# Kernel optimization log

Hardware: AMD Instinct MI355X
Metric: run time of the kernel (lower is better)

Reference implementation:

```python
import jax, jax.numpy as jnp
import numpy as np

B, S, D, H = 2, 2048, 1024, 16
DQ = D // H
EPS = 1e-5


def setup_inputs() -> dict:
    key = jax.random.key(0)
    ks = jax.random.split(key, 6)
    scale = 0.02
    return {
        "x": jax.random.normal(ks[0], (B, S, D), dtype=jnp.float32),
        "ln_g": jnp.ones((D,), dtype=jnp.float32),
        "ln_b": jnp.zeros((D,), dtype=jnp.float32),
        "Wq": jax.random.normal(ks[1], (D, D), dtype=jnp.float32) * scale,
        "bq": jnp.zeros((D,), dtype=jnp.float32),
        "Wk": jax.random.normal(ks[2], (D, D), dtype=jnp.float32) * scale,
        "bk": jnp.zeros((D,), dtype=jnp.float32),
        "Wv": jax.random.normal(ks[3], (D, D), dtype=jnp.float32) * scale,
        "bv": jnp.zeros((D,), dtype=jnp.float32),
        "Wo": jax.random.normal(ks[4], (D, D), dtype=jnp.float32) * scale,
        "bo": jnp.zeros((D,), dtype=jnp.float32),
    }


def reference(x, ln_g, ln_b, Wq, bq, Wk, bk, Wv, bv, Wo, bo):
    # pre-LayerNorm (torch default eps=1e-5, biased variance)
    mu = jnp.mean(x, axis=-1, keepdims=True)
    var = jnp.mean((x - mu) ** 2, axis=-1, keepdims=True)
    xn = (x - mu) * jax.lax.rsqrt(var + EPS) * ln_g + ln_b

    # QKV projections; weights stored [d_in, d_out]
    q = xn @ Wq + bq  # [B,S,D]
    k = xn @ Wk + bk
    v = xn @ Wv + bv

    # split heads -> [B,H,S,DQ]
    def heads(t):
        return t.reshape(B, S, H, DQ).transpose(0, 2, 1, 3)
    q, k, v = heads(q), heads(k), heads(v)

    scores = jnp.einsum("bhqd,bhkd->bhqk", q, k) / jnp.sqrt(jnp.float32(DQ))
    causal = jnp.tril(jnp.ones((S, S), dtype=bool))  # True = keep
    scores = jnp.where(causal, scores, -jnp.inf)
    probs = jax.nn.softmax(scores, axis=-1)
    attn = jnp.einsum("bhqk,bhkd->bhqd", probs, v)  # [B,H,S,DQ]

    # merge heads: [B,H,S,DQ] -> [B,S,H*DQ] (matches transpose/flatten/transpose)
    merged = attn.transpose(0, 2, 1, 3).reshape(B, S, D)
    out = merged @ Wo + bo
    return out + x
```

## Files before the change

kernel.cpp:

```cpp
#include <hip/hip_runtime.h>
#include <math.h>

#define BB 2
#define SS 2048
#define DD 1024
#define HH 16
#define DQK 64
#define NROWS (BB * SS)
#define NE ((size_t)BB * SS * DD)

using short8 = __attribute__((ext_vector_type(8))) short;
using f32x4  = __attribute__((ext_vector_type(4))) float;

__device__ __forceinline__ ushort f2bf(float f) {
  union { float f; unsigned u; } c; c.f = f;
  return (ushort)((c.u + 0x7fffu + ((c.u >> 16) & 1u)) >> 16);
}

__device__ __forceinline__ unsigned cvt_pk_bf16(float lo, float hi) {
  unsigned r;
  asm("v_cvt_pk_bf16_f32 %0, %1, %2" : "=v"(r) : "v"(lo), "v"(hi));
  return r;
}

__device__ __forceinline__ f32x4 mfma16(short8 a, short8 b, f32x4 c) {
  return __builtin_amdgcn_mfma_f32_16x16x32_bf16(a, b, c, 0, 0, 0);
}

typedef __attribute__((address_space(1))) const unsigned gas_u32;
typedef __attribute__((address_space(3))) unsigned las_u32;
__device__ __forceinline__ void gload_lds16(const void* g, void* l) {
  __builtin_amdgcn_global_load_lds((gas_u32*)g, (las_u32*)l, 16, 0, 0);
}

__global__ __launch_bounds__(256) void ln_fwd(const float* __restrict__ x,
                                              const float* __restrict__ g,
                                              const float* __restrict__ bta,
                                              ushort* __restrict__ xn) {
  const int row = blockIdx.x;
  const int t = threadIdx.x;
  float4 v = ((const float4*)(x + (size_t)row * DD))[t];
  float s  = v.x + v.y + v.z + v.w;
  float ss = v.x * v.x + v.y * v.y + v.z * v.z + v.w * v.w;
#pragma unroll
  for (int off = 32; off > 0; off >>= 1) {
    s  += __shfl_xor(s, off);
    ss += __shfl_xor(ss, off);
  }
  __shared__ float red[8];
  const int wid = t >> 6, lane = t & 63;
  if (lane == 0) { red[wid] = s; red[4 + wid] = ss; }
  __syncthreads();
  const float stot  = red[0] + red[1] + red[2] + red[3];
  const float sstot = red[4] + red[5] + red[6] + red[7];
  const float mu  = stot * (1.0f / DD);
  const float var = sstot * (1.0f / DD) - mu * mu;
  const float inv = rsqrtf(var + 1e-5f);
  const float4 g4 = ((const float4*)g)[t];
  const float4 b4 = ((const float4*)bta)[t];
  ushort4 o;
  o.x = f2bf((v.x - mu) * inv * g4.x + b4.x);
  o.y = f2bf((v.y - mu) * inv * g4.y + b4.y);
  o.z = f2bf((v.z - mu) * inv * g4.z + b4.z);
  o.w = f2bf((v.w - mu) * inv * g4.w + b4.w);
  ((ushort4*)(xn + (size_t)row * DD))[t] = o;
}

__global__ __launch_bounds__(256) void wtrans(const float* __restrict__ Wq,
                                              const float* __restrict__ Wk,
                                              const float* __restrict__ Wv,
                                              const float* __restrict__ Wo,
                                              ushort* __restrict__ wt) {
  const int z = blockIdx.z;
  const float* W = (z == 0) ? Wq : (z == 1) ? Wk : (z == 2) ? Wv : Wo;
  ushort* dst = wt + (size_t)z * DD * DD;
  __shared__ float tile[64][65];
  const int t = threadIdx.x;
  const int k0 = blockIdx.x * 64, n0 = blockIdx.y * 64;
  const int tr = t >> 4, tc = (t & 15) * 4;
#pragma unroll
  for (int rr = 0; rr < 64; rr += 16) {
    float4 v = *(const float4*)(W + (size_t)(k0 + rr + tr) * DD + n0 + tc);
    tile[rr + tr][tc + 0] = v.x;
    tile[rr + tr][tc + 1] = v.y;
    tile[rr + tr][tc + 2] = v.z;
    tile[rr + tr][tc + 3] = v.w;
  }
  __syncthreads();
#pragma unroll
  for (int rr = 0; rr < 64; rr += 16) {
    const int n = rr + tr;
    ushort4 o;
    o.x = f2bf(tile[tc + 0][n]);
    o.y = f2bf(tile[tc + 1][n]);
    o.z = f2bf(tile[tc + 2][n]);
    o.w = f2bf(tile[tc + 3][n]);
    *(ushort4*)(dst + (size_t)(n0 + n) * DD + k0 + tc) = o;
  }
}

#define GEMM_CORE(Ag, Bg)                                                     \
  f32x4 acc[4][4];                                                            \
  _Pragma("unroll")                                                           \
  for (int m = 0; m < 4; ++m)                                                 \
    _Pragma("unroll")                                                         \
    for (int n = 0; n < 4; ++n) acc[m][n] = (f32x4){0.f, 0.f, 0.f, 0.f};     \
  const int cs = ((t & 3) * 16) ^ (((t >> 2) & 3) * 16);                      \
  const int fsw = (r16 & 3) * 16;                                             \
  {                                                                           \
    GSTAGE(Ag, Bg, 0, 0);                                                     \
    int cur = 0;                                                              \
    for (int k0 = 0; k0 < DD; k0 += 32) {                                     \
      asm volatile("s_waitcnt vmcnt(0)" ::: "memory");                        \
      __syncthreads();                                                        \
      if (k0 + 32 < DD) GSTAGE(Ag, Bg, cur ^ 1, k0 + 32);                     \
      const char* Ac = (const char*)&As[cur][0][0];                           \
      const char* Bc = (const char*)&Bs[cur][0][0];                           \
      short8 af[4], bf[4];                                                    \
      _Pragma("unroll")                                                       \
      for (int m = 0; m < 4; ++m)                                             \
        af[m] = *(const short8*)(Ac + (wr * 64 + m * 16 + r16) * 64 +         \
                                 ((g * 16) ^ fsw));                           \
      _Pragma("unroll")                                                       \
      for (int n = 0; n < 4; ++n)                                             \
        bf[n] = *(const short8*)(Bc + (wc * 64 + n * 16 + r16) * 64 +         \
                                 ((g * 16) ^ fsw));                           \
      _Pragma("unroll")                                                       \
      for (int m = 0; m < 4; ++m)                                             \
        _Pragma("unroll")                                                     \
        for (int n = 0; n < 4; ++n) acc[m][n] = mfma16(af[m], bf[n], acc[m][n]); \
      cur ^= 1;                                                               \
    }                                                                         \
  }

#define GSTAGE(Ag, Bg, buf, k0)                                               \
  {                                                                           \
    _Pragma("unroll")                                                         \
    for (int i = 0; i < 2; ++i) {                                             \
      gload_lds16(Ag + (size_t)(row0 + i * 64 + (t >> 2)) * (DD * 2) +        \
                      (k0) * 2 + cs,                                          \
                  (char*)&As[buf][0][0] + i * 4096 + t * 16);                 \
      gload_lds16(Bg + (size_t)(col0 + i * 64 + (t >> 2)) * (DD * 2) +        \
                      (k0) * 2 + cs,                                          \
                  (char*)&Bs[buf][0][0] + i * 4096 + t * 16);                 \
    }                                                                         \
  }

__global__ __launch_bounds__(256) void gemm_qkv(
    const ushort* __restrict__ A, const ushort* __restrict__ wt,
    const float* __restrict__ bq, const float* __restrict__ bk,
    const float* __restrict__ bv, ushort* __restrict__ qb,
    ushort* __restrict__ kb, ushort* __restrict__ vt) {
  __shared__ ushort As[2][128][32];
  __shared__ ushort Bs[2][128][32];
  const int t = threadIdx.x;
  const int lane = t & 63;
  const int w = t >> 6, wr = w >> 1, wc = w & 1;
  const int r16 = lane & 15, g = lane >> 4;
  const int row0 = blockIdx.x * 128;
  const int mat = blockIdx.y >> 3;
  const int col0 = (blockIdx.y & 7) * 128;
  const char* Ag = (const char*)A;
  const char* Bg = (const char*)(wt + (size_t)mat * DD * DD);
  const float* bias = (mat == 0) ? bq : (mat == 1) ? bk : bv;
  const float scl = (mat == 0) ? 0.125f * 1.44269504f : 1.0f;

  GEMM_CORE(Ag, Bg)

#pragma unroll
  for (int n = 0; n < 4; ++n) {
    const int c = col0 + wc * 64 + n * 16 + r16;
    const float bc = bias[c];
#pragma unroll
    for (int m = 0; m < 4; ++m) {
      const int rbase = row0 + wr * 64 + m * 16 + g * 4;
      if (mat < 2) {
        ushort* outb = (mat == 0) ? qb : kb;
#pragma unroll
        for (int e = 0; e < 4; ++e)
          outb[(size_t)(rbase + e) * DD + c] = f2bf((acc[m][n][e] + bc) * scl);
      } else {
        uint2 st;
        st.x = cvt_pk_bf16(acc[m][n][0] + bc, acc[m][n][1] + bc);
        st.y = cvt_pk_bf16(acc[m][n][2] + bc, acc[m][n][3] + bc);
        const size_t vrow = (size_t)((rbase >> 11) * HH + (c >> 6)) * DQK + (c & 63);
        *(uint2*)(vt + vrow * SS + (rbase & 2047)) = st;
      }
    }
  }
}

__global__ __launch_bounds__(256) void gemm_o(
    const ushort* __restrict__ A, const ushort* __restrict__ Bt,
    const float* __restrict__ bias, const float* __restrict__ resid,
    float* __restrict__ outf) {
  __shared__ ushort As[2][128][32];
  __shared__ ushort Bs[2][128][32];
  const int t = threadIdx.x;
  const int lane = t & 63;
  const int w = t >> 6, wr = w >> 1, wc = w & 1;
  const int r16 = lane & 15, g = lane >> 4;
  const int row0 = blockIdx.x * 128;
  const int col0 = blockIdx.y * 128;
  const char* Ag = (const char*)A;
  const char* Bg = (const char*)Bt;

  GEMM_CORE(Ag, Bg)

#pragma unroll
  for (int n = 0; n < 4; ++n) {
    const int c = col0 + wc * 64 + n * 16 + r16;
    const float bc = bias[c];
#pragma unroll
    for (int m = 0; m < 4; ++m) {
      const int rbase = row0 + wr * 64 + m * 16 + g * 4;
#pragma unroll
      for (int e = 0; e < 4; ++e) {
        const size_t idx = (size_t)(rbase + e) * DD + c;
        outf[idx] = acc[m][n][e] + bc + resid[idx];
      }
    }
  }
}

__global__ __launch_bounds__(256) void attn_mfma(const ushort* __restrict__ Q,
                                                 const ushort* __restrict__ K,
                                                 const ushort* __restrict__ Vt,
                                                 ushort* __restrict__ O) {
  __shared__ ushort Ks[2][64][64];
  __shared__ ushort Vs[2][64][64];
  __shared__ ushort Ps[4][16][64];

  const int t = threadIdx.x, lane = t & 63, ww = t >> 6;
  const int r16 = lane & 15, g = lane >> 4;

  const int bid = blockIdx.x;
  const int xcd = bid & 7, idx = bid >> 3;
  const int bh = xcd * 4 + (idx & 3);
  const int qb = 31 - (idx >> 2);
  const int b = bh >> 4, h = bh & 15;
  const size_t tokbase = (size_t)b * SS;
  const size_t hoff = (size_t)h * DQK;
  const int q0 = qb * 64 + ww * 16;
  const int nt = qb + 1;

  const int srow = t >> 3;
  const int scol = (t & 7) * 16;
  const char* Kb = (const char*)(K + tokbase * DD + hoff);
  const char* Vb = (const char*)(Vt + (size_t)bh * DQK * SS);
  const int sw = (r16 & 7) << 4;

#define STAGE(buf, j0)                                                        \
  {                                                                           \
    _Pragma("unroll")                                                         \
    for (int i = 0; i < 2; ++i) {                                             \
      const int R = i * 32 + srow;                                            \
      const int Cs = scol ^ ((R & 7) << 4);                                   \
      gload_lds16(Kb + ((size_t)((j0) + R) * DD) * 2 + Cs,                    \
                  (char*)&Ks[buf][0][0] + i * 4096 + ww * 1024);              \
      gload_lds16(Vb + ((size_t)R * SS + (j0)) * 2 + Cs,                      \
                  (char*)&Vs[buf][0][0] + i * 4096 + ww * 1024);              \
    }                                                                         \
  }

  short8 qf[2];
#pragma unroll
  for (int kc = 0; kc < 2; ++kc)
    qf[kc] = *(const short8*)(Q + (tokbase + q0 + r16) * DD + hoff + kc * 32 + g * 8);

  f32x4 o[4];
#pragma unroll
  for (int dt = 0; dt < 4; ++dt) o[dt] = (f32x4){0.f, 0.f, 0.f, 0.f};
  float rm = -INFINITY, rl = 0.f;
  const int thr = q0 + r16 - g * 4;

  STAGE(0, 0);
  int cur = 0;
  for (int tt = 0; tt < nt; ++tt) {
    asm volatile("s_waitcnt vmcnt(0)" ::: "memory");
    __syncthreads();
    if (tt + 1 < nt) STAGE(cur ^ 1, (tt + 1) * 64);

    const char* Kc = (const char*)&Ks[cur][0][0];
    const char* Vc = (const char*)&Vs[cur][0][0];

    f32x4 s4[4];
    __builtin_amdgcn_s_setprio(1);
#pragma unroll
    for (int t2 = 0; t2 < 4; ++t2) {
      const int rb = (t2 * 16 + r16) * 128;
      const short8 k0 = *(const short8*)(Kc + rb + ((g * 16) ^ sw));
      const short8 k1 = *(const short8*)(Kc + rb + ((64 + g * 16) ^ sw));
      f32x4 s = mfma16(k0, qf[0], (f32x4){0.f, 0.f, 0.f, 0.f});
      s4[t2] = mfma16(k1, qf[1], s);
    }
    __builtin_amdgcn_s_setprio(0);

    if (tt == nt - 1) {
#pragma unroll
      for (int t2 = 0; t2 < 4; ++t2)
#pragma unroll
        for (int r = 0; r < 4; ++r)
          s4[t2][r] = (tt * 64 + t2 * 16 + r <= thr) ? s4[t2][r] : -INFINITY;
    }

    float mx = fmaxf(
        fmaxf(fmaxf(fmaxf(s4[0][0], s4[0][1]), fmaxf(s4[0][2], s4[0][3])),
              fmaxf(fmaxf(s4[1][0], s4[1][1]), fmaxf(s4[1][2], s4[1][3]))),
        fmaxf(fmaxf(fmaxf(s4[2][0], s4[2][1]), fmaxf(s4[2][2], s4[2][3])),
              fmaxf(fmaxf(s4[3][0], s4[3][1]), fmaxf(s4[3][2], s4[3][3]))));

    if (!__all(mx - rm <= 8.f)) {
      float mf = fmaxf(mx, __shfl_xor(mx, 16));
      mf = fmaxf(mf, __shfl_xor(mf, 32));
      const float mn = fmaxf(rm, mf);
      const float sc = __builtin_amdgcn_exp2f(rm - mn);
      rl *= sc;
#pragma unroll
      for (int dt = 0; dt < 4; ++dt) o[dt] *= sc;
      rm = mn;
    }

#pragma unroll
    for (int t2 = 0; t2 < 4; ++t2) {
      const float p0 = __builtin_amdgcn_exp2f(s4[t2][0] - rm);
      const float p1 = __builtin_amdgcn_exp2f(s4[t2][1] - rm);
      const float p2 = __builtin_amdgcn_exp2f(s4[t2][2] - rm);
      const float p3 = __builtin_amdgcn_exp2f(s4[t2][3] - rm);
      rl += (p0 + p1) + (p2 + p3);
      uint2 pk;
      pk.x = cvt_pk_bf16(p0, p1);
      pk.y = cvt_pk_bf16(p2, p3);
      *(uint2*)((char*)&Ps[ww][0][0] + r16 * 128 + ((t2 * 32 + g * 8) ^ sw)) = pk;
    }

    __builtin_amdgcn_s_setprio(1);
#pragma unroll
    for (int kc = 0; kc < 2; ++kc) {
      const short8 pb = *(const short8*)((const char*)&Ps[ww][0][0] + r16 * 128 +
                                         ((kc * 64 + g * 16) ^ sw));
#pragma unroll
      for (int dt = 0; dt < 4; ++dt) {
        const short8 vf = *(const short8*)(Vc + (dt * 16 + r16) * 128 +
                                           ((kc * 64 + g * 16) ^ sw));
        o[dt] = mfma16(vf, pb, o[dt]);
      }
    }
    __builtin_amdgcn_s_setprio(0);
    cur ^= 1;
  }
#undef STAGE

  rl += __shfl_xor(rl, 16);
  rl += __shfl_xor(rl, 32);
  const float inv = 1.0f / rl;
#pragma unroll
  for (int dt = 0; dt < 4; ++dt) {
    uint2 st;
    st.x = cvt_pk_bf16(o[dt][0] * inv, o[dt][1] * inv);
    st.y = cvt_pk_bf16(o[dt][2] * inv, o[dt][3] * inv);
    *(uint2*)(O + (tokbase + q0 + r16) * DD + hoff + dt * 16 + g * 4) = st;
  }
}

extern "C" void kernel_launch(void* const* d_in, const int* in_sizes, int n_in,
                              void* d_out, int out_size, void* d_ws, size_t ws_size,
                              hipStream_t stream) {
  const float* x    = (const float*)d_in[0];
  const float* ln_g = (const float*)d_in[1];
  const float* ln_b = (const float*)d_in[2];
  const float* Wq   = (const float*)d_in[3];
  const float* bq   = (const float*)d_in[4];
  const float* Wk   = (const float*)d_in[5];
  const float* bk   = (const float*)d_in[6];
  const float* Wv   = (const float*)d_in[7];
  const float* bv   = (const float*)d_in[8];
  const float* Wo   = (const float*)d_in[9];
  const float* bo   = (const float*)d_in[10];
  float* out = (float*)d_out;

  ushort* ws  = (ushort*)d_ws;
  ushort* xn  = ws;
  ushort* qb  = xn + NE;
  ushort* kb  = qb + NE;
  ushort* vt  = kb + NE;
  ushort* ab  = vt + NE;
  ushort* wt  = ab + NE;
  ushort* wot = wt + (size_t)3 * DD * DD;

  wtrans<<<dim3(16, 16, 4), 256, 0, stream>>>(Wq, Wk, Wv, Wo, wt);
  ln_fwd<<<NROWS, 256, 0, stream>>>(x, ln_g, ln_b, xn);

  gemm_qkv<<<dim3(NROWS / 128, 24), 256, 0, stream>>>(xn, wt, bq, bk, bv,
                                                      qb, kb, vt);

  attn_mfma<<<BB * HH * (SS / 64), 256, 0, stream>>>(qb, kb, vt, ab);

  gemm_o<<<dim3(NROWS / 128, DD / 128), 256, 0, stream>>>(ab, wot, bo, x, out);
}
```

Before: 118.8 us.

## Merge prep kernels, keep softmax probs in registers, rebalance causal attention blocks

Merges the LayerNorm and weight-transpose kernels into one launch that dispatches by block index. In attention, K rows are read in a permuted order so the QK^T accumulator layout lines up with the B-operand layout for the PV MFMA. This lets the bf16 probabilities be packed straight into registers and drops the per-wave LDS P buffer and its writes and reads. The query-block mapping is also interleaved so long and short causal tiles pair up across the launch order. The permuted key order requires a matching causal-mask index change, which is error-prone.

```diff
diff --git a/kernel.cpp b/kernel.cpp
--- a/kernel.cpp
+++ b/kernel.cpp
@@ -33,69 +33,69 @@
   __builtin_amdgcn_global_load_lds((gas_u32*)g, (las_u32*)l, 16, 0, 0);
 }
 
-__global__ __launch_bounds__(256) void ln_fwd(const float* __restrict__ x,
-                                              const float* __restrict__ g,
-                                              const float* __restrict__ bta,
-                                              ushort* __restrict__ xn) {
-  const int row = blockIdx.x;
-  const int t = threadIdx.x;
-  float4 v = ((const float4*)(x + (size_t)row * DD))[t];
-  float s  = v.x + v.y + v.z + v.w;
-  float ss = v.x * v.x + v.y * v.y + v.z * v.z + v.w * v.w;
-#pragma unroll
-  for (int off = 32; off > 0; off >>= 1) {
-    s  += __shfl_xor(s, off);
-    ss += __shfl_xor(ss, off);
-  }
-  __shared__ float red[8];
-  const int wid = t >> 6, lane = t & 63;
-  if (lane == 0) { red[wid] = s; red[4 + wid] = ss; }
-  __syncthreads();
-  const float stot  = red[0] + red[1] + red[2] + red[3];
-  const float sstot = red[4] + red[5] + red[6] + red[7];
-  const float mu  = stot * (1.0f / DD);
-  const float var = sstot * (1.0f / DD) - mu * mu;
-  const float inv = rsqrtf(var + 1e-5f);
-  const float4 g4 = ((const float4*)g)[t];
-  const float4 b4 = ((const float4*)bta)[t];
-  ushort4 o;
-  o.x = f2bf((v.x - mu) * inv * g4.x + b4.x);
-  o.y = f2bf((v.y - mu) * inv * g4.y + b4.y);
-  o.z = f2bf((v.z - mu) * inv * g4.z + b4.z);
-  o.w = f2bf((v.w - mu) * inv * g4.w + b4.w);
-  ((ushort4*)(xn + (size_t)row * DD))[t] = o;
-}
-
-__global__ __launch_bounds__(256) void wtrans(const float* __restrict__ Wq,
-                                              const float* __restrict__ Wk,
-                                              const float* __restrict__ Wv,
-                                              const float* __restrict__ Wo,
-                                              ushort* __restrict__ wt) {
-  const int z = blockIdx.z;
-  const float* W = (z == 0) ? Wq : (z == 1) ? Wk : (z == 2) ? Wv : Wo;
-  ushort* dst = wt + (size_t)z * DD * DD;
+__global__ __launch_bounds__(256) void prep(const float* __restrict__ x,
+                                            const float* __restrict__ g,
+                                            const float* __restrict__ bta,
+                                            ushort* __restrict__ xn,
+                                            const float* __restrict__ Wq,
+                                            const float* __restrict__ Wk,
+                                            const float* __restrict__ Wv,
+                                            const float* __restrict__ Wo,
+                                            ushort* __restrict__ wt) {
   __shared__ float tile[64][65];
   const int t = threadIdx.x;
-  const int k0 = blockIdx.x * 64, n0 = blockIdx.y * 64;
-  const int tr = t >> 4, tc = (t & 15) * 4;
-#pragma unroll
-  for (int rr = 0; rr < 64; rr += 16) {
-    float4 v = *(const float4*)(W + (size_t)(k0 + rr + tr) * DD + n0 + tc);
-    tile[rr + tr][tc + 0] = v.x;
-    tile[rr + tr][tc + 1] = v.y;
-    tile[rr + tr][tc + 2] = v.z;
-    tile[rr + tr][tc + 3] = v.w;
-  }
-  __syncthreads();
-#pragma unroll
-  for (int rr = 0; rr < 64; rr += 16) {
-    const int n = rr + tr;
+  if (blockIdx.x < NROWS) {
+    const int row = blockIdx.x;
+    float4 v = ((const float4*)(x + (size_t)row * DD))[t];
+    float s  = v.x + v.y + v.z + v.w;
+    float ss = v.x * v.x + v.y * v.y + v.z * v.z + v.w * v.w;
+#pragma unroll
+    for (int off = 32; off > 0; off >>= 1) {
+      s  += __shfl_xor(s, off);
+      ss += __shfl_xor(ss, off);
+    }
+    const int wid = t >> 6, lane = t & 63;
+    if (lane == 0) { tile[0][wid] = s; tile[0][4 + wid] = ss; }
+    __syncthreads();
+    const float stot  = tile[0][0] + tile[0][1] + tile[0][2] + tile[0][3];
+    const float sstot = tile[0][4] + tile[0][5] + tile[0][6] + tile[0][7];
+    const float mu  = stot * (1.0f / DD);
+    const float var = sstot * (1.0f / DD) - mu * mu;
+    const float inv = rsqrtf(var + 1e-5f);
+    const float4 g4 = ((const float4*)g)[t];
+    const float4 b4 = ((const float4*)bta)[t];
     ushort4 o;
-    o.x = f2bf(tile[tc + 0][n]);
-    o.y = f2bf(tile[tc + 1][n]);
-    o.z = f2bf(tile[tc + 2][n]);
-    o.w = f2bf(tile[tc + 3][n]);
-    *(ushort4*)(dst + (size_t)(n0 + n) * DD + k0 + tc) = o;
+    o.x = f2bf((v.x - mu) * inv * g4.x + b4.x);
+    o.y = f2bf((v.y - mu) * inv * g4.y + b4.y);
+    o.z = f2bf((v.z - mu) * inv * g4.z + b4.z);
+    o.w = f2bf((v.w - mu) * inv * g4.w + b4.w);
+    ((ushort4*)(xn + (size_t)row * DD))[t] = o;
+  } else {
+    const int wb = blockIdx.x - NROWS;
+    const int z = wb >> 8;
+    const int k0 = (wb & 15) * 64, n0 = ((wb >> 4) & 15) * 64;
+    const float* W = (z == 0) ? Wq : (z == 1) ? Wk : (z == 2) ? Wv : Wo;
+    ushort* dst = wt + (size_t)z * DD * DD;
+    const int tr = t >> 4, tc = (t & 15) * 4;
+#pragma unroll
+    for (int rr = 0; rr < 64; rr += 16) {
+      float4 v = *(const float4*)(W + (size_t)(k0 + rr + tr) * DD + n0 + tc);
+      tile[rr + tr][tc + 0] = v.x;
+      tile[rr + tr][tc + 1] = v.y;
+      tile[rr + tr][tc + 2] = v.z;
+      tile[rr + tr][tc + 3] = v.w;
+    }
+    __syncthreads();
+#pragma unroll
+    for (int rr = 0; rr < 64; rr += 16) {
+      const int n = rr + tr;
+      ushort4 o;
+      o.x = f2bf(tile[tc + 0][n]);
+      o.y = f2bf(tile[tc + 1][n]);
+      o.z = f2bf(tile[tc + 2][n]);
+      o.w = f2bf(tile[tc + 3][n]);
+      *(ushort4*)(dst + (size_t)(n0 + n) * DD + k0 + tc) = o;
+    }
   }
 }
 
@@ -229,15 +229,16 @@
                                                  ushort* __restrict__ O) {
   __shared__ ushort Ks[2][64][64];
   __shared__ ushort Vs[2][64][64];
-  __shared__ ushort Ps[4][16][64];
 
   const int t = threadIdx.x, lane = t & 63, ww = t >> 6;
   const int r16 = lane & 15, g = lane >> 4;
 
   const int bid = blockIdx.x;
-  const int xcd = bid & 7, idx = bid >> 3;
-  const int bh = xcd * 4 + (idx & 3);
-  const int qb = 31 - (idx >> 2);
+  const int xcd = bid & 7;
+  const int bh = xcd * 4 + ((bid >> 3) & 3);
+  const int m = (bid >> 5) & 7;
+  const int j = bid >> 8;
+  const int qb = (j == 0) ? (31 - m) : (j == 1) ? m : (j == 2) ? (23 - m) : (8 + m);
   const int b = bh >> 4, h = bh & 15;
   const size_t tokbase = (size_t)b * SS;
   const size_t hoff = (size_t)h * DQK;
@@ -249,6 +250,7 @@
   const char* Kb = (const char*)(K + tokbase * DD + hoff);
   const char* Vb = (const char*)(Vt + (size_t)bh * DQK * SS);
   const int sw = (r16 & 7) << 4;
+  const int rlo = (r16 & 3) + ((r16 >> 2) << 3);
 
 #define STAGE(buf, j0)                                                        \
   {                                                                           \
@@ -272,7 +274,6 @@
 #pragma unroll
   for (int dt = 0; dt < 4; ++dt) o[dt] = (f32x4){0.f, 0.f, 0.f, 0.f};
   float rm = -INFINITY, rl = 0.f;
-  const int thr = q0 + r16 - g * 4;
 
   STAGE(0, 0);
   int cur = 0;
@@ -288,20 +289,25 @@
     __builtin_amdgcn_s_setprio(1);
 #pragma unroll
     for (int t2 = 0; t2 < 4; ++t2) {
-      const int rb = (t2 * 16 + r16) * 128;
-      const short8 k0 = *(const short8*)(Kc + rb + ((g * 16) ^ sw));
-      const short8 k1 = *(const short8*)(Kc + rb + ((64 + g * 16) ^ sw));
+      const int kk = rlo + (t2 & 1) * 4 + (t2 >> 1) * 32;
+      const int sk = (kk & 7) << 4;
+      const int rb = kk * 128;
+      const short8 k0 = *(const short8*)(Kc + rb + ((g * 16) ^ sk));
+      const short8 k1 = *(const short8*)(Kc + rb + ((64 + g * 16) ^ sk));
       f32x4 s = mfma16(k0, qf[0], (f32x4){0.f, 0.f, 0.f, 0.f});
       s4[t2] = mfma16(k1, qf[1], s);
     }
     __builtin_amdgcn_s_setprio(0);
 
     if (tt == nt - 1) {
-#pragma unroll
-      for (int t2 = 0; t2 < 4; ++t2)
+      const int thrl = q0 + r16 - g * 8 - tt * 64;
+#pragma unroll
+      for (int t2 = 0; t2 < 4; ++t2) {
+        const int bb = (t2 & 1) * 4 + (t2 >> 1) * 32;
 #pragma unroll
         for (int r = 0; r < 4; ++r)
-          s4[t2][r] = (tt * 64 + t2 * 16 + r <= thr) ? s4[t2][r] : -INFINITY;
+          s4[t2][r] = (bb + r <= thrl) ? s4[t2][r] : -INFINITY;
+      }
     }
 
     float mx = fmaxf(
@@ -321,6 +327,7 @@
       rm = mn;
     }
 
+    union { unsigned u[4]; short8 s; } pbu[2];
 #pragma unroll
     for (int t2 = 0; t2 < 4; ++t2) {
       const float p0 = __builtin_amdgcn_exp2f(s4[t2][0] - rm);
@@ -328,22 +335,18 @@
       const float p2 = __builtin_amdgcn_exp2f(s4[t2][2] - rm);
       const float p3 = __builtin_amdgcn_exp2f(s4[t2][3] - rm);
       rl += (p0 + p1) + (p2 + p3);
-      uint2 pk;
-      pk.x = cvt_pk_bf16(p0, p1);
-      pk.y = cvt_pk_bf16(p2, p3);
-      *(uint2*)((char*)&Ps[ww][0][0] + r16 * 128 + ((t2 * 32 + g * 8) ^ sw)) = pk;
+      pbu[t2 >> 1].u[(t2 & 1) * 2 + 0] = cvt_pk_bf16(p0, p1);
+      pbu[t2 >> 1].u[(t2 & 1) * 2 + 1] = cvt_pk_bf16(p2, p3);
     }
 
     __builtin_amdgcn_s_setprio(1);
 #pragma unroll
     for (int kc = 0; kc < 2; ++kc) {
-      const short8 pb = *(const short8*)((const char*)&Ps[ww][0][0] + r16 * 128 +
-                                         ((kc * 64 + g * 16) ^ sw));
 #pragma unroll
       for (int dt = 0; dt < 4; ++dt) {
         const short8 vf = *(const short8*)(Vc + (dt * 16 + r16) * 128 +
                                            ((kc * 64 + g * 16) ^ sw));
-        o[dt] = mfma16(vf, pb, o[dt]);
+        o[dt] = mfma16(vf, pbu[kc].s, o[dt]);
       }
     }
     __builtin_amdgcn_s_setprio(0);
@@ -388,8 +391,7 @@
   ushort* wt  = ab + NE;
   ushort* wot = wt + (size_t)3 * DD * DD;
 
-  wtrans<<<dim3(16, 16, 4), 256, 0, stream>>>(Wq, Wk, Wv, Wo, wt);
-  ln_fwd<<<NROWS, 256, 0, stream>>>(x, ln_g, ln_b, xn);
+  prep<<<NROWS + 1024, 256, 0, stream>>>(x, ln_g, ln_b, xn, Wq, Wk, Wv, Wo, wt);
 
   gemm_qkv<<<dim3(NROWS / 128, 24), 256, 0, stream>>>(xn, wt, bq, bk, bv,
                                                       qb, kb, vt);
```

After: 115.0 us. 1.03x faster.
